# Kernel optimization log

Hardware: AMD Instinct MI355X
Metric: run time of the kernel (lower is better)

## Reference

```python
import jax, jax.numpy as jnp
import numpy as np

ANGRES = 5  # u = v = angRes, n = 25


def _l2norm(x, axis):
    n = jnp.sqrt(jnp.sum(x * x, axis=axis, keepdims=True))
    return x / jnp.maximum(n, 1e-12)  # matches torch F.normalize eps


def _cos_attn(qm, km, vm):
    # qm: (b, M, K), km: (b, K, M), vm: (b, M, K)
    q = _l2norm(qm, -1)
    k = _l2norm(km, -2)
    att = jax.nn.softmax(q @ k, axis=-1)  # (b, M, M)
    return att @ vm


def _af_attn(x, u, v):  # AngularFrequencyAttention: b c (u v) h w -> b (c u) (h v w)
    b, c, n, h, w = x.shape
    t = x.reshape(b, c, u, v, h, w)
    qm = t.transpose(0, 1, 2, 4, 3, 5).reshape(b, c * u, h * v * w)   # (b,c,u,h,v,w)
    km = t.transpose(0, 4, 3, 5, 1, 2).reshape(b, h * v * w, c * u)   # (b,h,v,w,c,u)
    o = _cos_attn(qm, km, qm)
    o = o.reshape(b, c, u, h, v, w).transpose(0, 1, 2, 4, 3, 5).reshape(b, c, n, h, w)
    return o + x


def _sa_attn(x, u, v):  # SpatialAngularAttention: b c (u v) h w -> b (h u) (c v w)
    b, c, n, h, w = x.shape
    t = x.reshape(b, c, u, v, h, w)
    qm = t.transpose(0, 4, 2, 1, 3, 5).reshape(b, h * u, c * v * w)   # (b,h,u,c,v,w)
    km = t.transpose(0, 1, 3, 5, 4, 2).reshape(b, c * v * w, h * u)   # (b,c,v,w,h,u)
    o = _cos_attn(qm, km, qm)
    o = o.reshape(b, h, u, c, v, w).transpose(0, 3, 2, 4, 1, 5).reshape(b, c, n, h, w)
    return o + x


def _sf_attn(x, u, v):  # SpatialFrequencyAttention: b c (u v) h w -> b (c h) (w u v)
    b, c, n, h, w = x.shape
    t = x.reshape(b, c, u, v, h, w)
    qm = t.transpose(0, 1, 4, 5, 2, 3).reshape(b, c * h, w * u * v)   # (b,c,h,w,u,v)
    km = t.transpose(0, 5, 2, 3, 1, 4).reshape(b, w * u * v, c * h)   # (b,w,u,v,c,h)
    o = _cos_attn(qm, km, qm)
    o = o.reshape(b, c, h, w, u, v).transpose(0, 1, 4, 5, 2, 3).reshape(b, c, n, h, w)
    return o + x


def _layernorm(x, g, bta, eps=1e-5):
    mu = jnp.mean(x, -1, keepdims=True)
    var = jnp.mean(jnp.square(x - mu), -1, keepdims=True)
    return (x - mu) * jax.lax.rsqrt(var + eps) * g + bta


def setup_inputs() -> dict:
    key = jax.random.key(0)
    k0, k1, k2 = jax.random.split(key, 3)
    b, c, n, h, w = 4, 64, 25, 48, 48
    x = jax.random.normal(k0, (b, c, n, h, w), dtype=jnp.float32)
    gamma = jnp.ones((3 * c,), dtype=jnp.float32)
    beta = jnp.zeros((3 * c,), dtype=jnp.float32)
    w1 = jax.random.normal(k1, (3 * c, c), dtype=jnp.float32) * 0.02
    w2 = jax.random.normal(k2, (c, c), dtype=jnp.float32) * 0.02
    return {"x": x, "gamma": gamma, "beta": beta, "w1": w1, "w2": w2}


def reference(x, gamma, beta, w1, w2):
    u = v = ANGRES
    b, c, n, h, w = x.shape
    sf = _sf_attn(x, u, v)
    af = _af_attn(x, u, v)
    sa = _sa_attn(x, u, v)
    cat = jnp.concatenate([sf, af, sa], axis=1)            # (b, 3c, n, h, w)
    f = cat.transpose(0, 3, 4, 2, 1).reshape(b * h * w, n, 3 * c)
    y = _layernorm(f, gamma, beta)
    y = jax.nn.relu(y @ w1) @ w2                            # (bhw, n, c); dropout p=0.01 is eval-identity
    out = y.reshape(b, h, w, n, c).transpose(0, 4, 3, 1, 2) + x
    return out
```

## Files before the change

### kernel.cpp

```cpp
#include <hip/hip_runtime.h>
#include <stdint.h>

typedef __attribute__((ext_vector_type(8))) short bf16x8;
typedef __attribute__((ext_vector_type(4))) float f32x4;

__device__ __forceinline__ float b2f(short s) {
  union { unsigned u; float f; } a; a.u = ((unsigned)(unsigned short)s) << 16; return a.f;
}
__device__ __forceinline__ short f2b(float f) {
  union { float f; unsigned u; } a; a.f = f;
  unsigned r = a.u + 0x7fffu + ((a.u >> 16) & 1u);
  return (short)(r >> 16);
}
__device__ __forceinline__ void gload16(const void* g, void* l) {
  __builtin_amdgcn_global_load_lds((__attribute__((address_space(1))) void*)g,
                                   (__attribute__((address_space(3))) void*)l, 16, 0, 0);
}

#define SWZ(row, col) ((col) ^ (((row) & 7) << 3))


__global__ __launch_bounds__(256) void permute_sf_k(const float* __restrict__ x, short* __restrict__ Q) {
  __shared__ float buf[4][1200];
  int wave = threadIdx.x >> 6, lane = threadIdx.x & 63;
  int gr = blockIdx.x * 4 + wave;
  int b = gr / 3072, m = gr - b * 3072;
  int c = m / 48, hh = m - c * 48;
  const float* xb = x + (long)(b * 64 + c) * 57600 + hh * 48;
  for (int uv = 0; uv < 25; ++uv)
    if (lane < 48) buf[wave][uv * 48 + lane] = xb[uv * 2304 + lane];
  __syncthreads();
  short* Qr = Q + (long)gr * 1280;
  for (int k = lane; k < 1280; k += 64) {
    float v = 0.f;
    if (k < 1200) { int wv = k / 25, uv = k - wv * 25; v = buf[wave][uv * 48 + wv]; }
    Qr[k] = f2b(v);
  }
}

template<int BR>
__global__ __launch_bounds__(256) void permtr_k(const float* __restrict__ x,
                                                short* __restrict__ Q, short* __restrict__ QT) {
  constexpr int M  = (BR == 1) ? 320 : 240;
  constexpr int Mp = (BR == 1) ? 384 : 256;
  constexpr int Kp = (BR == 1) ? 11520 : 15360;
  __shared__ short t[32][33];
  int b = blockIdx.z;
  int k0 = blockIdx.x * 32, m0 = blockIdx.y * 32;
  int tx = threadIdx.x & 31, ty = threadIdx.x >> 5;
  const float* xb = x + (long)b * 3686400;
  #pragma unroll
  for (int i = 0; i < 32; i += 8) {
    int m = m0 + ty + i, k = k0 + tx;
    float v = 0.f;
    if (m < M) {
      int q1 = k / 240, r2 = k - q1 * 240;
      int v5 = r2 / 48, wv = r2 - v5 * 48;
      int a1 = m / 5, u = m - a1 * 5;
      long xi;
      if (BR == 1) xi = ((long)a1 * 25 + u * 5 + v5) * 2304 + q1 * 48 + wv;
      else         xi = ((long)q1 * 25 + u * 5 + v5) * 2304 + a1 * 48 + wv;
      v = xb[xi];
    }
    t[ty + i][tx] = f2b(v);
  }
  __syncthreads();
  long Qb = (long)b * Mp * Kp;
  #pragma unroll
  for (int i = 0; i < 32; i += 8)
    Q[Qb + (long)(m0 + ty + i) * Kp + k0 + tx] = t[ty + i][tx];
  #pragma unroll
  for (int i = 0; i < 32; i += 8)
    QT[Qb + (long)(k0 + ty + i) * Mp + m0 + tx] = t[tx][ty + i];
}

__global__ __launch_bounds__(256) void transpose_k(const short* __restrict__ in, short* __restrict__ out,
                                                   int R, int C) {
  __shared__ short t[32][33];
  long base = (long)blockIdx.z * R * C;
  int c0 = blockIdx.x * 32, r0 = blockIdx.y * 32;
  int tx = threadIdx.x & 31, ty = threadIdx.x >> 5;
  #pragma unroll
  for (int i = 0; i < 32; i += 8)
    t[ty + i][tx] = in[base + (long)(r0 + ty + i) * C + c0 + tx];
  __syncthreads();
  #pragma unroll
  for (int i = 0; i < 32; i += 8)
    out[base + (long)(c0 + ty + i) * R + r0 + tx] = t[tx][ty + i];
}

__global__ __launch_bounds__(256) void invnorm_k(const short* __restrict__ Q, long sQ, int Kp,
                                                 int Mvalid, int Mp, float* __restrict__ inv) {
  __shared__ float red[256];
  int m = blockIdx.x, b = blockIdx.y, tid = threadIdx.x;
  float acc = 0.f;
  if (m < Mvalid) {
    const short* row = Q + (long)b * sQ + (long)m * Kp;
    for (int k = tid * 8; k < Kp; k += 2048) {
      bf16x8 v = *(const bf16x8*)&row[k];
      #pragma unroll
      for (int j = 0; j < 8; ++j) { float f = b2f(v[j]); acc += f * f; }
    }
  }
  red[tid] = acc; __syncthreads();
  #pragma unroll
  for (int s2 = 128; s2 > 0; s2 >>= 1) {
    if (tid < s2) red[tid] += red[tid + s2];
    __syncthreads();
  }
  if (tid == 0)
    inv[(long)b * Mp + m] = (m < Mvalid) ? 1.0f / fmaxf(sqrtf(red[0]), 1e-12f) : 1.0f;
}

__global__ __launch_bounds__(256, 2) void gemm1_tri_k(const short* __restrict__ Q,
                                                      const float* __restrict__ invn,
                                                      short* __restrict__ att,
                                                      float* __restrict__ rowsum) {
  __shared__ short sm[32768];
  int tid = threadIdx.x, wave = tid >> 6, lane = tid & 63;
  int la = lane & 15, lb = lane >> 4;
  int bat = blockIdx.z;
  int bx = blockIdx.x, yt = 0, rem = bx;
  while (rem >= 24 - yt) { rem -= 24 - yt; ++yt; }
  int xt = yt + rem;
  const short* Qb = Q + (long)bat * 3932160L;
  const float* inv = invn + (long)bat * 3072;
  int row0 = yt * 128, col0 = xt * 128;
  f32x4 acc[4][4] = {};
  int wr = wave >> 1, wc = wave & 1;
  int rloc = tid >> 3, cbase = (tid & 7) * 8;
  int ldsoff = tid * 8;

  const short *pA[4], *pB[4];
  #pragma unroll
  for (int p = 0; p < 4; ++p) {
    int row = p * 32 + rloc;
    int sc = SWZ(row, cbase);
    pA[p] = Qb + (long)(row0 + row) * 1280 + sc;
    pB[p] = Qb + (long)(col0 + row) * 1280 + sc;
  }

  #define TRI_STAGE(KT, BUF) { \
    short* Asb = sm + (BUF) * 16384; \
    short* Bsb = Asb + 8192; \
    _Pragma("unroll") \
    for (int p = 0; p < 4; ++p) { \
      gload16(pA[p] + (KT) * 64, (void*)(Asb + p * 2048 + ldsoff)); \
      gload16(pB[p] + (KT) * 64, (void*)(Bsb + p * 2048 + ldsoff)); \
    } }
  #define TRI_COMP(BUF) { \
    const short* Asb = sm + (BUF) * 16384; \
    const short* Bsb = Asb + 8192; \
    _Pragma("unroll") \
    for (int kk = 0; kk < 64; kk += 32) { \
      bf16x8 av[4], bv[4]; \
      _Pragma("unroll") \
      for (int m = 0; m < 4; ++m) \
        av[m] = *(const bf16x8*)&Asb[(wr * 64 + m * 16 + la) * 64 + SWZ(la, kk + lb * 8)]; \
      _Pragma("unroll") \
      for (int nn = 0; nn < 4; ++nn) \
        bv[nn] = *(const bf16x8*)&Bsb[(wc * 64 + nn * 16 + la) * 64 + SWZ(la, kk + lb * 8)]; \
      _Pragma("unroll") \
      for (int m = 0; m < 4; ++m) \
        _Pragma("unroll") \
        for (int nn = 0; nn < 4; ++nn) \
          acc[m][nn] = __builtin_amdgcn_mfma_f32_16x16x32_bf16(av[m], bv[nn], acc[m][nn], 0, 0, 0); \
    } }

  TRI_STAGE(0, 0)
  for (int kt = 0; kt < 19; ++kt) {
    TRI_STAGE(kt + 1, (kt + 1) & 1)
    asm volatile("s_waitcnt vmcnt(8)" ::: "memory");
    __builtin_amdgcn_s_barrier();
    TRI_COMP(kt & 1)
    asm volatile("" ::: "memory");
    __builtin_amdgcn_s_barrier();
  }
  asm volatile("s_waitcnt vmcnt(0)" ::: "memory");
  __builtin_amdgcn_s_barrier();
  TRI_COMP(1)
  asm volatile("" ::: "memory");
  __builtin_amdgcn_s_barrier();

  short* staged = sm;
  #pragma unroll
  for (int m = 0; m < 4; ++m) {
    #pragma unroll
    for (int nn = 0; nn < 4; ++nn) {
      int cl = wc * 64 + nn * 16 + la;
      float ic = inv[col0 + cl];
      #pragma unroll
      for (int j = 0; j < 4; ++j) {
        int rl = wr * 64 + m * 16 + lb * 4 + j;
        staged[rl * 136 + cl] = f2b(__expf(acc[m][nn][j] * inv[row0 + rl] * ic));
      }
    }
  }
  __syncthreads();
  short* attb = att + (long)bat * 9437184L;
  float* rsb = rowsum + (long)bat * 3072;
  {
    int r = tid >> 1, half = tid & 1;
    short* dst = attb + (long)(row0 + r) * 3072 + col0 + half * 64;
    const short* src = &staged[r * 136 + half * 64];
    float s = 0.f;
    #pragma unroll
    for (int q = 0; q < 8; ++q) {
      bf16x8 v = *(const bf16x8*)&src[q * 8];
      *(bf16x8*)&dst[q * 8] = v;
      #pragma unroll
      for (int jj = 0; jj < 8; ++jj) s += b2f(v[jj]);
    }
    s += __shfl_xor(s, 1, 64);
    if (half == 0) atomicAdd(&rsb[row0 + r], s);
  }
  if (xt != yt) {
    int c = tid >> 1, half = tid & 1;
    short* dst = attb + (long)(col0 + c) * 3072 + row0 + half * 64;
    float s = 0.f;
    #pragma unroll
    for (int q = 0; q < 8; ++q) {
      bf16x8 o;
      #pragma unroll
      for (int jj = 0; jj < 8; ++jj) {
        o[jj] = staged[(half * 64 + q * 8 + jj) * 136 + c];
        s += b2f(o[jj]);
      }
      *(bf16x8*)&dst[q * 8] = o;
    }
    s += __shfl_xor(s, 1, 64);
    if (half == 0) atomicAdd(&rsb[col0 + c], s);
  }
}

__global__ __launch_bounds__(256, 2) void gemm_s_k(
    const short* __restrict__ A, long sA, int lda,
    int ktotal, int ksper, int SK,
    float* __restrict__ Sf, long sS, int ldc)
{
  __shared__ short sm[32768];
  int tid = threadIdx.x;
  int wave = tid >> 6, lane = tid & 63;
  int la = lane & 15, lb = lane >> 4;
  int bz = blockIdx.z;
  int bat = bz / SK, kc = bz - bat * SK;
  int row0 = blockIdx.y * 128, col0 = blockIdx.x * 128;
  const short* Ab = A + (long)bat * sA;
  int kb = kc * ksper, ke = min(ktotal, kb + ksper);
  int L = ke - kb;
  f32x4 acc[4][4] = {};
  int wr = wave >> 1, wc = wave & 1;
  int rloc = tid >> 3, cbase = (tid & 7) * 8;
  int ldsoff = tid * 8;

  const short *pA[4], *pB[4];
  #pragma unroll
  for (int p = 0; p < 4; ++p) {
    int row = p * 32 + rloc;
    int sc = SWZ(row, cbase);
    pA[p] = Ab + (long)(row0 + row) * lda + sc;
    pB[p] = Ab + (long)(col0 + row) * lda + sc;
  }

  #define GS_STAGE(KT, BUF) { \
    short* Asb = sm + (BUF) * 16384; \
    short* Bsb = Asb + 8192; \
    _Pragma("unroll") \
    for (int p = 0; p < 4; ++p) { \
      gload16(pA[p] + (KT) * 64, (void*)(Asb + p * 2048 + ldsoff)); \
      gload16(pB[p] + (KT) * 64, (void*)(Bsb + p * 2048 + ldsoff)); \
    } }
  #define GS_COMP(BUF) { \
    const short* Asb = sm + (BUF) * 16384; \
    const short* Bsb = Asb + 8192; \
    _Pragma("unroll") \
    for (int kk = 0; kk < 64; kk += 32) { \
      bf16x8 av[4], bv[4]; \
      _Pragma("unroll") \
      for (int m = 0; m < 4; ++m) \
        av[m] = *(const bf16x8*)&Asb[(wr * 64 + m * 16 + la) * 64 + SWZ(la, kk + lb * 8)]; \
      _Pragma("unroll") \
      for (int nn = 0; nn < 4; ++nn) \
        bv[nn] = *(const bf16x8*)&Bsb[(wc * 64 + nn * 16 + la) * 64 + SWZ(la, kk + lb * 8)]; \
      _Pragma("unroll") \
      for (int m = 0; m < 4; ++m) \
        _Pragma("unroll") \
        for (int nn = 0; nn < 4; ++nn) \
          acc[m][nn] = __builtin_amdgcn_mfma_f32_16x16x32_bf16(av[m], bv[nn], acc[m][nn], 0, 0, 0); \
    } }

  GS_STAGE(kb, 0)
  for (int t = 0; t < L - 1; ++t) {
    GS_STAGE(kb + t + 1, (t + 1) & 1)
    asm volatile("s_waitcnt vmcnt(8)" ::: "memory");
    __builtin_amdgcn_s_barrier();
    GS_COMP(t & 1)
    asm volatile("" ::: "memory");
    __builtin_amdgcn_s_barrier();
  }
  asm volatile("s_waitcnt vmcnt(0)" ::: "memory");
  __builtin_amdgcn_s_barrier();
  GS_COMP((L - 1) & 1)

  float* Sb = Sf + (long)bat * sS;
  #pragma unroll
  for (int m = 0; m < 4; ++m) {
    int gr0 = row0 + wr * 64 + m * 16 + lb * 4;
    #pragma unroll
    for (int nn = 0; nn < 4; ++nn) {
      int gc = col0 + wc * 64 + nn * 16 + la;
      #pragma unroll
      for (int j = 0; j < 4; ++j)
        atomicAdd(&Sb[(long)(gr0 + j) * ldc + gc], acc[m][nn][j]);
    }
  }
}

__global__ __launch_bounds__(256) void softmax_k(const float* __restrict__ Sf, long sS,
                                                 const float* __restrict__ inv,
                                                 int Mvalid, int Mp,
                                                 short* __restrict__ att, long sAtt) {
  __shared__ float srow[3072];
  __shared__ float red[256];
  int row = blockIdx.x, b = blockIdx.y, tid = threadIdx.x;
  const float* Sr = Sf + (long)b * sS + (long)row * Mp;
  const float* invb = inv + (long)b * Mp;
  float inv_i = invb[row];
  float sum = 0.f;
  for (int j = tid; j < Mvalid; j += 256) {
    float e = __expf(Sr[j] * inv_i * invb[j]);
    srow[j] = e; sum += e;
  }
  red[tid] = sum; __syncthreads();
  #pragma unroll
  for (int s2 = 128; s2 > 0; s2 >>= 1) {
    if (tid < s2) red[tid] += red[tid + s2];
    __syncthreads();
  }
  float rden = 1.0f / red[0];
  short* ar = att + (long)b * sAtt + (long)row * Mp;
  for (int j = tid; j < Mp; j += 256)
    ar[j] = (j < Mvalid) ? f2b(srow[j] * rden) : (short)0;
}

__global__ __launch_bounds__(256, 2) void gemm2sf_k(const short* __restrict__ A,
                                                    const short* __restrict__ B,
                                                    const float* __restrict__ rowsum,
                                                    short* __restrict__ F) {
  __shared__ short sm[32768];
  int tid = threadIdx.x, wave = tid >> 6, lane = tid & 63;
  int la = lane & 15, lb = lane >> 4;
  int wr = wave >> 1, wc = wave & 1;
  int wk;
  { int xcd = blockIdx.x & 7, j = blockIdx.x >> 3; wk = xcd * 120 + j; }
  int yt = wk % 24, rem = wk / 24;
  int xt = rem % 10, bat = rem / 10;
  const short* Ab = A + (long)bat * 9437184L;
  const short* Bb = B + (long)bat * 3932160L;
  int rloc = tid >> 3, cbase = (tid & 7) * 8;
  int ldsoff = tid * 8;
  f32x4 acc[4][4] = {};

  const short *pA[4], *pB[4];
  #pragma unroll
  for (int p = 0; p < 4; ++p) {
    int row = p * 32 + rloc;
    int sc = SWZ(row, cbase);
    int rga = (row & 63) * 48 + yt * 2 + (row >> 6);
    pA[p] = Ab + (long)rga * 3072 + sc;
    int rgb = xt * 128 + row;
    pB[p] = Bb + (long)rgb * 3072 + sc;
  }

  #define G2_STAGE(KT, BUF) { \
    short* Asb = sm + (BUF) * 16384; \
    short* Bsb = Asb + 8192; \
    _Pragma("unroll") \
    for (int p = 0; p < 4; ++p) { \
      gload16(pA[p] + (KT) * 64, (void*)(Asb + p * 2048 + ldsoff)); \
      gload16(pB[p] + (KT) * 64, (void*)(Bsb + p * 2048 + ldsoff)); \
    } }
  #define G2_COMP(BUF) { \
    const short* Asb = sm + (BUF) * 16384; \
    const short* Bsb = Asb + 8192; \
    _Pragma("unroll") \
    for (int kk = 0; kk < 64; kk += 32) { \
      bf16x8 av[4], bv[4]; \
      _Pragma("unroll") \
      for (int m = 0; m < 4; ++m) \
        av[m] = *(const bf16x8*)&Asb[(wr * 64 + m * 16 + la) * 64 + SWZ(la, kk + lb * 8)]; \
      _Pragma("unroll") \
      for (int nn = 0; nn < 4; ++nn) \
        bv[nn] = *(const bf16x8*)&Bsb[(wc * 64 + nn * 16 + la) * 64 + SWZ(la, kk + lb * 8)]; \
      _Pragma("unroll") \
      for (int m = 0; m < 4; ++m) \
        _Pragma("unroll") \
        for (int nn = 0; nn < 4; ++nn) \
          acc[m][nn] = __builtin_amdgcn_mfma_f32_16x16x32_bf16(av[m], bv[nn], acc[m][nn], 0, 0, 0); \
    } }

  G2_STAGE(0, 0)
  for (int kt = 0; kt < 47; ++kt) {
    G2_STAGE(kt + 1, (kt + 1) & 1)
    asm volatile("s_waitcnt vmcnt(8)" ::: "memory");
    __builtin_amdgcn_s_barrier();
    G2_COMP(kt & 1)
    asm volatile("" ::: "memory");
    __builtin_amdgcn_s_barrier();
  }
  asm volatile("s_waitcnt vmcnt(0)" ::: "memory");
  __builtin_amdgcn_s_barrier();
  G2_COMP(1)
  asm volatile("" ::: "memory");
  __builtin_amdgcn_s_barrier();

  const float* rsb = rowsum + (long)bat * 3072;
  float rs[4][4];
  #pragma unroll
  for (int m = 0; m < 4; ++m)
    #pragma unroll
    for (int j = 0; j < 4; ++j)
      rs[m][j] = 1.0f / rsb[(m * 16 + lb * 4 + j) * 48 + yt * 2 + wr];

  short* staged = sm;
  #pragma unroll
  for (int m = 0; m < 4; ++m) {
    #pragma unroll
    for (int nn = 0; nn < 4; ++nn) {
      int cc = wc * 64 + nn * 16 + la;
      short4 o;
      o.x = f2b(acc[m][nn][0] * rs[m][0]); o.y = f2b(acc[m][nn][1] * rs[m][1]);
      o.z = f2b(acc[m][nn][2] * rs[m][2]); o.w = f2b(acc[m][nn][3] * rs[m][3]);
      *(short4*)&staged[(cc * 2 + wr) * 72 + m * 16 + lb * 4] = o;
    }
  }
  __syncthreads();
  #pragma unroll
  for (int rd = 0; rd < 8; ++rd) {
    int chunk = rd * 32 + (tid >> 3);
    int part = tid & 7;
    bf16x8 v = *(const bf16x8*)&staged[chunk * 72 + part * 8];
    int cc = chunk >> 1, sub = chunk & 1;
    int gc = xt * 128 + cc;
    if (gc < 1200) {
      int hh = yt * 2 + sub;
      int wv = gc / 25, nidx = gc - wv * 25;
      long base = (((long)(bat * 48 + hh) * 48 + wv) * 25 + nidx) * 192 + part * 8;
      *(bf16x8*)&F[base] = v;
    }
  }
}

template<int BR>
__global__ __launch_bounds__(256) void gemm2_k(const short* __restrict__ A,
                                               const short* __restrict__ B,
                                               short* __restrict__ F) {
  constexpr int NX  = (BR == 2) ? 45 : 60;
  constexpr int NY  = (BR == 2) ? 5 : 4;
  constexpr int NWG = NX * NY * 4;
  constexpr int LDA = (BR == 2) ? 384 : 256;
  constexpr long SA = (BR == 2) ? 147456L : 65536L;
  constexpr long SB = (BR == 2) ? 4423680L : 3932160L;
  constexpr int KST = (BR == 2) ? 6 : 4;

  __shared__ short sm[20480];
  short* As = sm;
  short* Bs = sm + 4096;
  int tid = threadIdx.x, wave = tid >> 6, lane = tid & 63;
  int la = lane & 15, lb = lane >> 4;

  int wk;
  { constexpr int q = NWG / 8, r = NWG % 8;
    int xcd = blockIdx.x & 7, j = blockIdx.x >> 3;
    wk = (xcd < r) ? xcd * (q + 1) + j : r * (q + 1) + (xcd - r) * q + j; }
  int yt = wk % NY, rem = wk / NY;
  int xt = rem % NX, bat = rem / NX;

  const short* Ab = A + (long)bat * SA;
  const short* Bb = B + (long)bat * SB;
  f32x4 acc[4][4] = {};
  int rloc = tid >> 3, cbase = (tid & 7) * 8;

  for (int kt = 0; kt < KST; ++kt) {
    int k0 = kt * 64;
    #pragma unroll
    for (int p = 0; p < 2; ++p) {
      int r = p * 32 + rloc;
      int sc = SWZ(r, cbase);
      int e = p * 2048 + tid * 8;
      int rowg = (BR == 2) ? (r * 5 + yt) : (yt * 64 + r);
      gload16(Ab + (long)rowg * LDA + k0 + sc, (void*)(As + e));
    }
    #pragma unroll
    for (int p = 0; p < 8; ++p) {
      int rb = p * 32 + rloc;
      int sc = SWZ(rb, cbase);
      int e = p * 2048 + tid * 8;
      int rowg;
      if (BR == 3) { int c = rb & 63, g = rb >> 6; rowg = c * 240 + xt * 4 + g; }
      else rowg = xt * 256 + rb;
      gload16(Bb + (long)rowg * LDA + k0 + sc, (void*)(Bs + e));
    }
    __syncthreads();
    #pragma unroll
    for (int kk = 0; kk < 64; kk += 32) {
      bf16x8 av[4], bv[4];
      #pragma unroll
      for (int m = 0; m < 4; ++m)
        av[m] = *(const bf16x8*)&As[(m * 16 + la) * 64 + SWZ(la, kk + lb * 8)];
      #pragma unroll
      for (int nn = 0; nn < 4; ++nn)
        bv[nn] = *(const bf16x8*)&Bs[(wave * 64 + nn * 16 + la) * 64 + SWZ(la, kk + lb * 8)];
      #pragma unroll
      for (int m = 0; m < 4; ++m)
        #pragma unroll
        for (int nn = 0; nn < 4; ++nn)
          acc[m][nn] = __builtin_amdgcn_mfma_f32_16x16x32_bf16(av[m], bv[nn], acc[m][nn], 0, 0, 0);
    }
    __syncthreads();
  }

  short* staged = sm;
  #pragma unroll
  for (int m = 0; m < 4; ++m) {
    #pragma unroll
    for (int nn = 0; nn < 4; ++nn) {
      if (BR == 3) {
        #pragma unroll
        for (int j = 0; j < 4; ++j)
          staged[((m * 16 + lb * 4 + j) * 4 + wave) * 72 + nn * 16 + la] = f2b(acc[m][nn][j]);
      } else {
        short4 o;
        o.x = f2b(acc[m][nn][0]); o.y = f2b(acc[m][nn][1]);
        o.z = f2b(acc[m][nn][2]); o.w = f2b(acc[m][nn][3]);
        *(short4*)&staged[(wave * 64 + nn * 16 + la) * 72 + m * 16 + lb * 4] = o;
      }
    }
  }
  __syncthreads();

  #pragma unroll
  for (int rd = 0; rd < 8; ++rd) {
    int chunk = rd * 32 + (tid >> 3);
    int part = tid & 7;
    bf16x8 v = *(const bf16x8*)&staged[chunk * 72 + part * 8];
    long base; bool ok = true;
    if (BR == 2) {
      int gc = xt * 256 + chunk;
      int hh = gc / 240, r2 = gc - hh * 240, v5 = r2 / 48, wv = r2 - v5 * 48;
      base = (((long)(bat * 48 + hh) * 48 + wv) * 25 + yt * 5 + v5) * 192 + 64 + part * 8;
    } else {
      int r = chunk >> 2, g = chunk & 3;
      int gr = yt * 64 + r; ok = (gr < 240);
      int hh = gr / 5, u = gr - hh * 5;
      int r2 = xt * 4 + g, v5 = r2 / 48, wv = r2 - v5 * 48;
      base = (((long)(bat * 48 + hh) * 48 + wv) * 25 + u * 5 + v5) * 192 + 128 + part * 8;
    }
    if (ok) *(bf16x8*)&F[base] = v;
  }
}

__global__ __launch_bounds__(256) void prep_w_k(const float* __restrict__ w1, const float* __restrict__ w2,
                                                short* __restrict__ w1t, short* __restrict__ w2t) {
  int idx = blockIdx.x * 256 + threadIdx.x;
  if (idx < 12288) {
    int i = idx / 64, j = idx - i * 64;
    w1t[j * 192 + i] = f2b(w1[idx]);
  } else if (idx < 16384) {
    int k = idx - 12288;
    int i = k / 64, j = k - i * 64;
    w2t[j * 64 + i] = f2b(w2[k]);
  }
}

__global__ __launch_bounds__(256) void ln_mlp_mfma_k(
    const short* __restrict__ F, const float* __restrict__ x,
    const float* __restrict__ gamma, const float* __restrict__ beta,
    const short* __restrict__ w1t, const short* __restrict__ w2t,
    float* __restrict__ out)
{
  int n = blockIdx.x, hh = blockIdx.y, b = blockIdx.z;
  __shared__ short A1[48 * 200];
  __shared__ float xs[64 * 49];
  __shared__ __align__(16) char pool[19584];
  short* Fs = (short*)pool;
  short* Y1 = (short*)pool;
  float* Y2 = (float*)(pool + 6912);
  int tid = threadIdx.x, wave = tid >> 6, lane = tid & 63;
  int la = lane & 15, lb = lane >> 4;
  long Fb0 = ((long)(b * 48 + hh) * 1200 + n) * 192;
  long xb = (long)b * 3686400 + (long)n * 2304 + hh * 48;

  #pragma unroll
  for (int it = 0; it < 5; ++it) {
    int ci = tid + 256 * it;
    if (ci < 1152) {
      int r = ci / 24, q = ci - r * 24;
      *(bf16x8*)&Fs[r * 192 + q * 8] = *(const bf16x8*)&F[Fb0 + (long)r * 4800 + q * 8];
    }
  }
  {
    int ch = tid >> 2, qq = tid & 3;
    const float* xr = x + xb + (long)ch * 57600 + qq * 12;
    #pragma unroll
    for (int i = 0; i < 12; ++i) xs[ch * 49 + qq * 12 + i] = xr[i];
  }
  __syncthreads();

  float g0 = gamma[lane], g1 = gamma[lane + 64], g2 = gamma[lane + 128];
  float bt0 = beta[lane], bt1 = beta[lane + 64], bt2 = beta[lane + 128];
  #pragma unroll 4
  for (int rr = 0; rr < 12; ++rr) {
    int r = wave * 12 + rr;
    float xv = xs[lane * 49 + r];
    float v0 = b2f(Fs[r * 192 + lane]) + xv;
    float v1 = b2f(Fs[r * 192 + lane + 64]) + xv;
    float v2 = b2f(Fs[r * 192 + lane + 128]) + xv;
    float s = v0 + v1 + v2;
    #pragma unroll
    for (int o = 32; o >= 1; o >>= 1) s += __shfl_xor(s, o, 64);
    float mu = s * (1.f / 192.f);
    float d0 = v0 - mu, d1 = v1 - mu, d2 = v2 - mu;
    float q = d0 * d0 + d1 * d1 + d2 * d2;
    #pragma unroll
    for (int o = 32; o >= 1; o >>= 1) q += __shfl_xor(q, o, 64);
    float rs = rsqrtf(q * (1.f / 192.f) + 1e-5f);
    A1[r * 200 + lane]       = f2b(d0 * rs * g0 + bt0);
    A1[r * 200 + lane + 64]  = f2b(d1 * rs * g1 + bt1);
    A1[r * 200 + lane + 128] = f2b(d2 * rs * g2 + bt2);
  }
  __syncthreads();

  f32x4 acc1[3] = {};
  #pragma unroll
  for (int ks = 0; ks < 6; ++ks) {
    bf16x8 bv = *(const bf16x8*)&w1t[(wave * 16 + la) * 192 + ks * 32 + lb * 8];
    #pragma unroll
    for (int m = 0; m < 3; ++m) {
      bf16x8 av = *(const bf16x8*)&A1[(m * 16 + la) * 200 + ks * 32 + lb * 8];
      acc1[m] = __builtin_amdgcn_mfma_f32_16x16x32_bf16(av, bv, acc1[m], 0, 0, 0);
    }
  }
  #pragma unroll
  for (int m = 0; m < 3; ++m)
    #pragma unroll
    for (int j = 0; j < 4; ++j)
      Y1[(m * 16 + lb * 4 + j) * 72 + wave * 16 + la] = f2b(fmaxf(acc1[m][j], 0.f));
  __syncthreads();

  f32x4 acc2[3] = {};
  #pragma unroll
  for (int ks = 0; ks < 2; ++ks) {
    bf16x8 bv = *(const bf16x8*)&w2t[(wave * 16 + la) * 64 + ks * 32 + lb * 8];
    #pragma unroll
    for (int m = 0; m < 3; ++m) {
      bf16x8 av = *(const bf16x8*)&Y1[(m * 16 + la) * 72 + ks * 32 + lb * 8];
      acc2[m] = __builtin_amdgcn_mfma_f32_16x16x32_bf16(av, bv, acc2[m], 0, 0, 0);
    }
  }
  #pragma unroll
  for (int m = 0; m < 3; ++m)
    #pragma unroll
    for (int j = 0; j < 4; ++j)
      Y2[(m * 16 + lb * 4 + j) * 66 + wave * 16 + la] = acc2[m][j];
  __syncthreads();

  #pragma unroll
  for (int i = 0; i < 12; ++i) {
    int e = tid + 256 * i;
    int cc = e / 48, wv = e - cc * 48;
    out[xb + (long)cc * 57600 + wv] = Y2[wv * 66 + cc] + xs[cc * 49 + wv];
  }
}

extern "C" void kernel_launch(void* const* d_in, const int* in_sizes, int n_in,
                              void* d_out, int out_size, void* d_ws, size_t ws_size,
                              hipStream_t stream) {
  (void)in_sizes; (void)n_in; (void)out_size;
  const float* x     = (const float*)d_in[0];
  const float* gamma = (const float*)d_in[1];
  const float* beta  = (const float*)d_in[2];
  const float* w1    = (const float*)d_in[3];
  const float* w2    = (const float*)d_in[4];
  float* out = (float*)d_out;

  const size_t NEED = 237191168UL;
  if (ws_size < NEED) return;
  char* ws = (char*)d_ws;
  short* F     = (short*)(ws);
  short* att   = (short*)(ws + 88473600UL);
  short* Qbf   = (short*)(ws + 163971072UL);
  short* QbfT  = (short*)(ws + 199360512UL);
  float* Sf    = (float*)(ws + 234749952UL);
  float* invn  = (float*)(ws + 237109248UL);
  short* w1t   = (short*)(ws + 237158400UL);
  short* w2t   = (short*)(ws + 237182976UL);

  prep_w_k<<<64, 256, 0, stream>>>(w1, w2, w1t, w2t);

  permute_sf_k<<<3072, 256, 0, stream>>>(x, Qbf);
  transpose_k<<<dim3(40, 96, 4), 256, 0, stream>>>(Qbf, QbfT, 3072, 1280);
  invnorm_k<<<dim3(3072, 4), 256, 0, stream>>>(Qbf, 3932160L, 1280, 3072, 3072, invn);
  hipMemsetAsync(Sf, 0, 49152, stream);
  gemm1_tri_k<<<dim3(300, 1, 4), 256, 0, stream>>>(Qbf, invn, att, Sf);
  gemm2sf_k<<<dim3(960), 256, 0, stream>>>(att, QbfT, Sf, F);

  permtr_k<1><<<dim3(360, 12, 4), 256, 0, stream>>>(x, Qbf, QbfT);
  invnorm_k<<<dim3(384, 4), 256, 0, stream>>>(Qbf, 4423680L, 11520, 320, 384, invn);
  hipMemsetAsync(Sf, 0, (size_t)4 * 384 * 384 * 4, stream);
  gemm_s_k<<<dim3(3, 3, 32), 256, 0, stream>>>(Qbf, 4423680L, 11520, 180, 23, 8, Sf, 147456L, 384);
  softmax_k<<<dim3(320, 4), 256, 0, stream>>>(Sf, 147456L, invn, 320, 384, att, 147456L);
  gemm2_k<2><<<dim3(900), 256, 0, stream>>>(att, QbfT, F);

  permtr_k<2><<<dim3(480, 8, 4), 256, 0, stream>>>(x, Qbf, QbfT);
  invnorm_k<<<dim3(256, 4), 256, 0, stream>>>(Qbf, 3932160L, 15360, 240, 256, invn);
  hipMemsetAsync(Sf, 0, (size_t)4 * 256 * 256 * 4, stream);
  gemm_s_k<<<dim3(2, 2, 64), 256, 0, stream>>>(Qbf, 3932160L, 15360, 240, 15, 16, Sf, 65536L, 256);
  softmax_k<<<dim3(240, 4), 256, 0, stream>>>(Sf, 65536L, invn, 240, 256, att, 65536L);
  gemm2_k<3><<<dim3(960), 256, 0, stream>>>(att, QbfT, F);

  ln_mlp_mfma_k<<<dim3(25, 48, 4), 256, 0, stream>>>(F, x, gamma, beta, w1t, w2t, out);
}
```

Before: 502.4 us.

## Merge AF and SA branch kernels and fold row norms into permute passes

Runs the AF and SA attention branches as single combined launches for permute/transpose, score GEMM, softmax and output GEMM, using separate workspace buffers so both branches coexist. The separate invnorm kernels are removed: squared row norms are now accumulated inside the permute kernels, with atomics for AF/SA and a wave reduction for SF. Softmax switches to one wave per row held in registers instead of a block-wide shared-memory reduction. The aim is fewer launches, less re-reading of Q for norms, and better occupancy from concurrent branch work. In exchange it adds runtime branching on block index, more atomics, and a larger live workspace footprint.

```diff
diff --git a/kernel.cpp b/kernel.cpp
--- a/kernel.cpp
+++ b/kernel.cpp
@@ -19,8 +19,9 @@
 
 #define SWZ(row, col) ((col) ^ (((row) & 7) << 3))
 
-
-__global__ __launch_bounds__(256) void permute_sf_k(const float* __restrict__ x, short* __restrict__ Q) {
+__global__ __launch_bounds__(256) void permute_sf_k(const float* __restrict__ x,
+                                                    short* __restrict__ Q,
+                                                    float* __restrict__ inv) {
   __shared__ float buf[4][1200];
   int wave = threadIdx.x >> 6, lane = threadIdx.x & 63;
   int gr = blockIdx.x * 4 + wave;
@@ -31,22 +32,32 @@
     if (lane < 48) buf[wave][uv * 48 + lane] = xb[uv * 2304 + lane];
   __syncthreads();
   short* Qr = Q + (long)gr * 1280;
+  float ss = 0.f;
   for (int k = lane; k < 1280; k += 64) {
     float v = 0.f;
     if (k < 1200) { int wv = k / 25, uv = k - wv * 25; v = buf[wave][uv * 48 + wv]; }
+    ss += v * v;
     Qr[k] = f2b(v);
   }
-}
-
-template<int BR>
-__global__ __launch_bounds__(256) void permtr_k(const float* __restrict__ x,
-                                                short* __restrict__ Q, short* __restrict__ QT) {
-  constexpr int M  = (BR == 1) ? 320 : 240;
-  constexpr int Mp = (BR == 1) ? 384 : 256;
-  constexpr int Kp = (BR == 1) ? 11520 : 15360;
+  #pragma unroll
+  for (int o = 32; o >= 1; o >>= 1) ss += __shfl_xor(ss, o, 64);
+  if (lane == 0) inv[gr] = 1.0f / fmaxf(sqrtf(ss), 1e-12f);
+}
+
+__global__ __launch_bounds__(256) void permtr_all_k(const float* __restrict__ x,
+    short* __restrict__ Qaf, short* __restrict__ QTaf,
+    short* __restrict__ Qsa, short* __restrict__ QTsa,
+    float* __restrict__ ssaf, float* __restrict__ sssa) {
   __shared__ short t[32][33];
-  int b = blockIdx.z;
-  int k0 = blockIdx.x * 32, m0 = blockIdx.y * 32;
+  int bid = blockIdx.x;
+  int isAF = (bid < 17280);
+  int M, Mp, Kp, kt, mt, b;
+  short *Q, *QT; float* ss;
+  if (isAF) { M = 320; Mp = 384; Kp = 11520; kt = bid % 360; int r = bid / 360; mt = r % 12; b = r / 12;
+              Q = Qaf; QT = QTaf; ss = ssaf; }
+  else { int id = bid - 17280; M = 240; Mp = 256; Kp = 15360; kt = id % 480; int r = id / 480; mt = r % 8; b = r / 8;
+         Q = Qsa; QT = QTsa; ss = sssa; }
+  int k0 = kt * 32, m0 = mt * 32;
   int tx = threadIdx.x & 31, ty = threadIdx.x >> 5;
   const float* xb = x + (long)b * 3686400;
   #pragma unroll
@@ -57,9 +68,8 @@
       int q1 = k / 240, r2 = k - q1 * 240;
       int v5 = r2 / 48, wv = r2 - v5 * 48;
       int a1 = m / 5, u = m - a1 * 5;
-      long xi;
-      if (BR == 1) xi = ((long)a1 * 25 + u * 5 + v5) * 2304 + q1 * 48 + wv;
-      else         xi = ((long)q1 * 25 + u * 5 + v5) * 2304 + a1 * 48 + wv;
+      long xi = isAF ? ((long)a1 * 25 + u * 5 + v5) * 2304 + q1 * 48 + wv
+                     : ((long)q1 * 25 + u * 5 + v5) * 2304 + a1 * 48 + wv;
       v = xb[xi];
     }
     t[ty + i][tx] = f2b(v);
@@ -72,6 +82,12 @@
   #pragma unroll
   for (int i = 0; i < 32; i += 8)
     QT[Qb + (long)(k0 + ty + i) * Mp + m0 + tx] = t[tx][ty + i];
+  if (threadIdx.x < 32 && m0 + (int)threadIdx.x < M) {
+    float s = 0.f;
+    #pragma unroll
+    for (int k = 0; k < 32; ++k) { float f = b2f(t[threadIdx.x][k]); s += f * f; }
+    atomicAdd(&ss[b * Mp + m0 + threadIdx.x], s);
+  }
 }
 
 __global__ __launch_bounds__(256) void transpose_k(const short* __restrict__ in, short* __restrict__ out,
@@ -87,29 +103,6 @@
   #pragma unroll
   for (int i = 0; i < 32; i += 8)
     out[base + (long)(c0 + ty + i) * R + r0 + tx] = t[tx][ty + i];
-}
-
-__global__ __launch_bounds__(256) void invnorm_k(const short* __restrict__ Q, long sQ, int Kp,
-                                                 int Mvalid, int Mp, float* __restrict__ inv) {
-  __shared__ float red[256];
-  int m = blockIdx.x, b = blockIdx.y, tid = threadIdx.x;
-  float acc = 0.f;
-  if (m < Mvalid) {
-    const short* row = Q + (long)b * sQ + (long)m * Kp;
-    for (int k = tid * 8; k < Kp; k += 2048) {
-      bf16x8 v = *(const bf16x8*)&row[k];
-      #pragma unroll
-      for (int j = 0; j < 8; ++j) { float f = b2f(v[j]); acc += f * f; }
-    }
-  }
-  red[tid] = acc; __syncthreads();
-  #pragma unroll
-  for (int s2 = 128; s2 > 0; s2 >>= 1) {
-    if (tid < s2) red[tid] += red[tid + s2];
-    __syncthreads();
-  }
-  if (tid == 0)
-    inv[(long)b * Mp + m] = (m < Mvalid) ? 1.0f / fmaxf(sqrtf(red[0]), 1e-12f) : 1.0f;
 }
 
 __global__ __launch_bounds__(256, 2) void gemm1_tri_k(const short* __restrict__ Q,
@@ -233,18 +226,32 @@
   }
 }
 
-__global__ __launch_bounds__(256, 2) void gemm_s_k(
-    const short* __restrict__ A, long sA, int lda,
-    int ktotal, int ksper, int SK,
-    float* __restrict__ Sf, long sS, int ldc)
+__global__ __launch_bounds__(256, 2) void gemm_s_all_k(
+    const short* __restrict__ Aaf, const short* __restrict__ Asa,
+    float* __restrict__ Sfaf, float* __restrict__ Sfsa)
 {
   __shared__ short sm[32768];
+  int bid = blockIdx.x;
+  const short* A; float* Sf;
+  int lda, ktotal, ksper, ldc, row0, col0, bat, kc;
+  long sA, sS;
+  if (bid < 288) {
+    int txy = bid % 9, z = bid / 9;
+    col0 = (txy % 3) * 128; row0 = (txy / 3) * 128;
+    bat = z / 8; kc = z % 8;
+    lda = 11520; ktotal = 180; ksper = 23; ldc = 384;
+    sA = 4423680L; sS = 147456L; A = Aaf; Sf = Sfaf;
+  } else {
+    int id = bid - 288;
+    int txy = id % 4, z = id / 4;
+    col0 = (txy % 2) * 128; row0 = (txy / 2) * 128;
+    bat = z / 16; kc = z % 16;
+    lda = 15360; ktotal = 240; ksper = 15; ldc = 256;
+    sA = 3932160L; sS = 65536L; A = Asa; Sf = Sfsa;
+  }
   int tid = threadIdx.x;
   int wave = tid >> 6, lane = tid & 63;
   int la = lane & 15, lb = lane >> 4;
-  int bz = blockIdx.z;
-  int bat = bz / SK, kc = bz - bat * SK;
-  int row0 = blockIdx.y * 128, col0 = blockIdx.x * 128;
   const short* Ab = A + (long)bat * sA;
   int kb = kc * ksper, ke = min(ktotal, kb + ksper);
   int L = ke - kb;
@@ -316,31 +323,39 @@
   }
 }
 
-__global__ __launch_bounds__(256) void softmax_k(const float* __restrict__ Sf, long sS,
-                                                 const float* __restrict__ inv,
-                                                 int Mvalid, int Mp,
-                                                 short* __restrict__ att, long sAtt) {
-  __shared__ float srow[3072];
-  __shared__ float red[256];
-  int row = blockIdx.x, b = blockIdx.y, tid = threadIdx.x;
+__global__ __launch_bounds__(256) void softmax_all_k(
+    const float* __restrict__ Sfaf, const float* __restrict__ Sfsa,
+    const float* __restrict__ ssaf, const float* __restrict__ sssa,
+    short* __restrict__ attaf, short* __restrict__ attsa)
+{
+  int wave = threadIdx.x >> 6, lane = threadIdx.x & 63;
+  int rid = blockIdx.x * 4 + wave;
+  int row, b, Mv, Mp; const float *Sf, *ss; short* att;
+  if (rid < 1280) { row = rid % 320; b = rid / 320; Mv = 320; Mp = 384; Sf = Sfaf; ss = ssaf; att = attaf; }
+  else { int id = rid - 1280; row = id % 240; b = id / 240; Mv = 240; Mp = 256; Sf = Sfsa; ss = sssa; att = attsa; }
+  long sS = (long)Mp * Mp;
   const float* Sr = Sf + (long)b * sS + (long)row * Mp;
-  const float* invb = inv + (long)b * Mp;
-  float inv_i = invb[row];
+  const float* ssb = ss + b * Mp;
+  float inv_i = rsqrtf(fmaxf(ssb[row], 1e-24f));
+  float ev[6] = {0.f, 0.f, 0.f, 0.f, 0.f, 0.f};
   float sum = 0.f;
-  for (int j = tid; j < Mvalid; j += 256) {
-    float e = __expf(Sr[j] * inv_i * invb[j]);
-    srow[j] = e; sum += e;
-  }
-  red[tid] = sum; __syncthreads();
-  #pragma unroll
-  for (int s2 = 128; s2 > 0; s2 >>= 1) {
-    if (tid < s2) red[tid] += red[tid + s2];
-    __syncthreads();
-  }
-  float rden = 1.0f / red[0];
-  short* ar = att + (long)b * sAtt + (long)row * Mp;
-  for (int j = tid; j < Mp; j += 256)
-    ar[j] = (j < Mvalid) ? f2b(srow[j] * rden) : (short)0;
+  #pragma unroll
+  for (int q = 0; q < 6; ++q) {
+    int j = q * 64 + lane;
+    if (j < Mv) {
+      float e = __expf(Sr[j] * inv_i * rsqrtf(fmaxf(ssb[j], 1e-24f)));
+      ev[q] = e; sum += e;
+    }
+  }
+  #pragma unroll
+  for (int o = 32; o >= 1; o >>= 1) sum += __shfl_xor(sum, o, 64);
+  float rden = 1.0f / sum;
+  short* ar = att + (long)b * sS + (long)row * Mp;
+  #pragma unroll
+  for (int q = 0; q < 6; ++q) {
+    int j = q * 64 + lane;
+    if (j < Mp) ar[j] = (j < Mv) ? f2b(ev[q] * rden) : (short)0;
+  }
 }
 
 __global__ __launch_bounds__(256, 2) void gemm2sf_k(const short* __restrict__ A,
@@ -451,56 +466,55 @@
   }
 }
 
-template<int BR>
-__global__ __launch_bounds__(256) void gemm2_k(const short* __restrict__ A,
-                                               const short* __restrict__ B,
-                                               short* __restrict__ F) {
-  constexpr int NX  = (BR == 2) ? 45 : 60;
-  constexpr int NY  = (BR == 2) ? 5 : 4;
-  constexpr int NWG = NX * NY * 4;
-  constexpr int LDA = (BR == 2) ? 384 : 256;
-  constexpr long SA = (BR == 2) ? 147456L : 65536L;
-  constexpr long SB = (BR == 2) ? 4423680L : 3932160L;
-  constexpr int KST = (BR == 2) ? 6 : 4;
-
+__global__ __launch_bounds__(256) void gemm2_afsa_k(
+    const short* __restrict__ attaf, const short* __restrict__ QTaf,
+    const short* __restrict__ attsa, const short* __restrict__ QTsa,
+    short* __restrict__ F)
+{
   __shared__ short sm[20480];
   short* As = sm;
   short* Bs = sm + 4096;
+  int bid = blockIdx.x;
+  int isAF = (bid < 900);
+  int NX, NY, LDA, KST, wk;
+  const short *A, *B; long SA, SB;
+  if (isAF) { NX = 45; NY = 5; LDA = 384; KST = 6; SA = 147456L; SB = 4423680L; A = attaf; B = QTaf; wk = bid; }
+  else { NX = 60; NY = 4; LDA = 256; KST = 4; SA = 65536L; SB = 3932160L; A = attsa; B = QTsa; wk = bid - 900; }
+  int yt = wk % NY, rem = wk / NY;
+  int xt = rem % NX, bat = rem / NX;
   int tid = threadIdx.x, wave = tid >> 6, lane = tid & 63;
   int la = lane & 15, lb = lane >> 4;
-
-  int wk;
-  { constexpr int q = NWG / 8, r = NWG % 8;
-    int xcd = blockIdx.x & 7, j = blockIdx.x >> 3;
-    wk = (xcd < r) ? xcd * (q + 1) + j : r * (q + 1) + (xcd - r) * q + j; }
-  int yt = wk % NY, rem = wk / NY;
-  int xt = rem % NX, bat = rem / NX;
-
   const short* Ab = A + (long)bat * SA;
   const short* Bb = B + (long)bat * SB;
   f32x4 acc[4][4] = {};
   int rloc = tid >> 3, cbase = (tid & 7) * 8;
+  int ldsoff = tid * 8;
+
+  const short *pA[2], *pB[8];
+  #pragma unroll
+  for (int p = 0; p < 2; ++p) {
+    int r = p * 32 + rloc;
+    int sc = SWZ(r, cbase);
+    int rowg = isAF ? (r * 5 + yt) : (yt * 64 + r);
+    pA[p] = Ab + (long)rowg * LDA + sc;
+  }
+  #pragma unroll
+  for (int p = 0; p < 8; ++p) {
+    int rb = p * 32 + rloc;
+    int sc = SWZ(rb, cbase);
+    int rowg;
+    if (isAF) rowg = xt * 256 + rb;
+    else { int c = rb & 63, g = rb >> 6; rowg = c * 240 + xt * 4 + g; }
+    pB[p] = Bb + (long)rowg * LDA + sc;
+  }
 
   for (int kt = 0; kt < KST; ++kt) {
-    int k0 = kt * 64;
-    #pragma unroll
-    for (int p = 0; p < 2; ++p) {
-      int r = p * 32 + rloc;
-      int sc = SWZ(r, cbase);
-      int e = p * 2048 + tid * 8;
-      int rowg = (BR == 2) ? (r * 5 + yt) : (yt * 64 + r);
-      gload16(Ab + (long)rowg * LDA + k0 + sc, (void*)(As + e));
-    }
-    #pragma unroll
-    for (int p = 0; p < 8; ++p) {
-      int rb = p * 32 + rloc;
-      int sc = SWZ(rb, cbase);
-      int e = p * 2048 + tid * 8;
-      int rowg;
-      if (BR == 3) { int c = rb & 63, g = rb >> 6; rowg = c * 240 + xt * 4 + g; }
-      else rowg = xt * 256 + rb;
-      gload16(Bb + (long)rowg * LDA + k0 + sc, (void*)(Bs + e));
-    }
+    #pragma unroll
+    for (int p = 0; p < 2; ++p)
+      gload16(pA[p] + kt * 64, (void*)(As + p * 2048 + ldsoff));
+    #pragma unroll
+    for (int p = 0; p < 8; ++p)
+      gload16(pB[p] + kt * 64, (void*)(Bs + p * 2048 + ldsoff));
     __syncthreads();
     #pragma unroll
     for (int kk = 0; kk < 64; kk += 32) {
@@ -525,7 +539,7 @@
   for (int m = 0; m < 4; ++m) {
     #pragma unroll
     for (int nn = 0; nn < 4; ++nn) {
-      if (BR == 3) {
+      if (!isAF) {
         #pragma unroll
         for (int j = 0; j < 4; ++j)
           staged[((m * 16 + lb * 4 + j) * 4 + wave) * 72 + nn * 16 + la] = f2b(acc[m][nn][j]);
@@ -545,7 +559,7 @@
     int part = tid & 7;
     bf16x8 v = *(const bf16x8*)&staged[chunk * 72 + part * 8];
     long base; bool ok = true;
-    if (BR == 2) {
+    if (isAF) {
       int gc = xt * 256 + chunk;
       int hh = gc / 240, r2 = gc - hh * 240, v5 = r2 / 48, wv = r2 - v5 * 48;
       base = (((long)(bat * 48 + hh) * 48 + wv) * 25 + yt * 5 + v5) * 192 + 64 + part * 8;
@@ -688,36 +702,39 @@
   if (ws_size < NEED) return;
   char* ws = (char*)d_ws;
   short* F     = (short*)(ws);
-  short* att   = (short*)(ws + 88473600UL);
-  short* Qbf   = (short*)(ws + 163971072UL);
-  short* QbfT  = (short*)(ws + 199360512UL);
-  float* Sf    = (float*)(ws + 234749952UL);
+  short* attsf = (short*)(ws + 88473600UL);
+  short* Qsf   = (short*)(ws + 163971072UL);
+  short* QTsf  = (short*)(ws + 199360512UL);
+  float* rowsum = (float*)(ws + 234749952UL);
   float* invn  = (float*)(ws + 237109248UL);
   short* w1t   = (short*)(ws + 237158400UL);
   short* w2t   = (short*)(ws + 237182976UL);
+  short* Qaf   = (short*)(ws + 88473600UL);
+  short* QTaf  = (short*)(ws + 123863040UL);
+  float* Sfsa  = (float*)(ws + 159252480UL);
+  float* ssaf  = (float*)(ws + 160301056UL);
+  float* sssa  = (float*)(ws + 160307200UL);
+  short* attaf = (short*)(ws + 160311296UL);
+  short* attsa = (short*)(ws + 161490944UL);
+  short* Qsa   = (short*)(ws + 163971072UL);
+  short* QTsa  = (short*)(ws + 195428352UL);
+  float* Sfaf  = (float*)(ws + 234749952UL);
 
   prep_w_k<<<64, 256, 0, stream>>>(w1, w2, w1t, w2t);
 
-  permute_sf_k<<<3072, 256, 0, stream>>>(x, Qbf);
-  transpose_k<<<dim3(40, 96, 4), 256, 0, stream>>>(Qbf, QbfT, 3072, 1280);
-  invnorm_k<<<dim3(3072, 4), 256, 0, stream>>>(Qbf, 3932160L, 1280, 3072, 3072, invn);
-  hipMemsetAsync(Sf, 0, 49152, stream);
-  gemm1_tri_k<<<dim3(300, 1, 4), 256, 0, stream>>>(Qbf, invn, att, Sf);
-  gemm2sf_k<<<dim3(960), 256, 0, stream>>>(att, QbfT, Sf, F);
-
-  permtr_k<1><<<dim3(360, 12, 4), 256, 0, stream>>>(x, Qbf, QbfT);
-  invnorm_k<<<dim3(384, 4), 256, 0, stream>>>(Qbf, 4423680L, 11520, 320, 384, invn);
-  hipMemsetAsync(Sf, 0, (size_t)4 * 384 * 384 * 4, stream);
-  gemm_s_k<<<dim3(3, 3, 32), 256, 0, stream>>>(Qbf, 4423680L, 11520, 180, 23, 8, Sf, 147456L, 384);
-  softmax_k<<<dim3(320, 4), 256, 0, stream>>>(Sf, 147456L, invn, 320, 384, att, 147456L);
-  gemm2_k<2><<<dim3(900), 256, 0, stream>>>(att, QbfT, F);
-
-  permtr_k<2><<<dim3(480, 8, 4), 256, 0, stream>>>(x, Qbf, QbfT);
-  invnorm_k<<<dim3(256, 4), 256, 0, stream>>>(Qbf, 3932160L, 15360, 240, 256, invn);
-  hipMemsetAsync(Sf, 0, (size_t)4 * 256 * 256 * 4, stream);
-  gemm_s_k<<<dim3(2, 2, 64), 256, 0, stream>>>(Qbf, 3932160L, 15360, 240, 15, 16, Sf, 65536L, 256);
-  softmax_k<<<dim3(240, 4), 256, 0, stream>>>(Sf, 65536L, invn, 240, 256, att, 65536L);
-  gemm2_k<3><<<dim3(960), 256, 0, stream>>>(att, QbfT, F);
+  permute_sf_k<<<3072, 256, 0, stream>>>(x, Qsf, invn);
+  transpose_k<<<dim3(40, 96, 4), 256, 0, stream>>>(Qsf, QTsf, 3072, 1280);
+  hipMemsetAsync(rowsum, 0, 49152, stream);
+  gemm1_tri_k<<<dim3(300, 1, 4), 256, 0, stream>>>(Qsf, invn, attsf, rowsum);
+  gemm2sf_k<<<dim3(960), 256, 0, stream>>>(attsf, QTsf, rowsum, F);
+
+  hipMemsetAsync(Sfaf, 0, 2359296, stream);
+  hipMemsetAsync(Sfsa, 0, 1048576, stream);
+  hipMemsetAsync(ssaf, 0, 10240, stream);
+  permtr_all_k<<<32640, 256, 0, stream>>>(x, Qaf, QTaf, Qsa, QTsa, ssaf, sssa);
+  gemm_s_all_k<<<544, 256, 0, stream>>>(Qaf, Qsa, Sfaf, Sfsa);
+  softmax_all_k<<<560, 256, 0, stream>>>(Sfaf, Sfsa, ssaf, sssa, attaf, attsa);
+  gemm2_afsa_k<<<1860, 256, 0, stream>>>(attaf, QTaf, attsa, QTsa, F);
 
   ln_mlp_mfma_k<<<dim3(25, 48, 4), 256, 0, stream>>>(F, x, gamma, beta, w1t, w2t, out);
 }
```

After: 519.9 us. 1.03x slower.
